# Optimization experiments

Measured on AMD Instinct MI355X. Metric: run time of the kernel, lower is better.

The kernel has to match this reference:

```python
import jax, jax.numpy as jnp
import numpy as np

Q, B, D = 512, 4, 1024      # qlen, batch, d_model
L, H, DH, DI = 4, 16, 64, 4096  # layers, heads, d_head, d_inner
M = 512                      # mem_len


def setup_inputs() -> dict:
    key = jax.random.key(0)
    ks = jax.random.split(key, 10)
    w = lambda i, shape: jax.random.normal(ks[i], shape, jnp.float32) * 0.02
    return dict(
        x=jax.random.normal(ks[0], (Q, B, D), jnp.float32),
        mems=jax.random.normal(ks[1], (L, M, B, D), jnp.float32),
        u=w(2, (H, DH)),
        v=w(3, (H, DH)),
        W_qkv=w(4, (L, D, 3 * H * DH)),
        W_o=w(5, (L, H * DH, D)),
        W_r=w(6, (L, D, H * DH)),
        ln1_g=jnp.ones((L, D), jnp.float32),
        ln1_b=jnp.zeros((L, D), jnp.float32),
        W1=w(7, (L, D, DI)),
        b1=jnp.zeros((L, DI), jnp.float32),
        W2=w(8, (L, DI, D)),
        b2=jnp.zeros((L, D), jnp.float32),
        ln2_g=jnp.ones((L, D), jnp.float32),
        ln2_b=jnp.zeros((L, D), jnp.float32),
    )


def _layer_norm(x, g, b):
    mu = x.mean(-1, keepdims=True)
    var = ((x - mu) ** 2).mean(-1, keepdims=True)
    return (x - mu) * jax.lax.rsqrt(var + 1e-5) * g + b


def _rel_shift(x):
    # x: [q, k, b, n] -> Transformer-XL relative shift
    q, k, b, n = x.shape
    x = jnp.pad(x, ((0, 0), (1, 0), (0, 0), (0, 0)))
    return x.reshape(k + 1, q, b, n)[1:].reshape(q, k, b, n)


def _pos_emb(klen, d):
    pos = jnp.arange(klen - 1, -1, -1.0, dtype=jnp.float32)
    inv_freq = 1.0 / (10000.0 ** (jnp.arange(0, d, 2, dtype=jnp.float32) / d))
    ang = pos[:, None] * inv_freq[None, :]
    return jnp.concatenate([jnp.sin(ang), jnp.cos(ang)], axis=-1)  # [klen, d]


def reference(x, mems, u, v, W_qkv, W_o, W_r, ln1_g, ln1_b, W1, b1, W2, b2, ln2_g, ln2_b):
    q_len, bsz, d = x.shape
    mlen = mems.shape[1]
    klen = mlen + q_len
    r = _pos_emb(klen, d)                       # [klen, d]
    scale = 1.0 / np.sqrt(DH)
    # causal mask with memory: query i may attend key j iff j - i <= mlen
    mask = (jnp.arange(klen)[None, :] - jnp.arange(q_len)[:, None]) > mlen  # [q, k]
    h = x
    for i in range(L):
        cat = jnp.concatenate([mems[i], h], axis=0)       # [klen, b, d]
        heads = cat @ W_qkv[i]                            # [klen, b, 3*H*DH]
        qh, kh, vh = jnp.split(heads, 3, axis=-1)
        qh = qh[-q_len:].reshape(q_len, bsz, H, DH)
        kh = kh.reshape(klen, bsz, H, DH)
        vh = vh.reshape(klen, bsz, H, DH)
        rk = (r @ W_r[i]).reshape(klen, H, DH)            # [klen, H, DH]
        AC = jnp.einsum('ibnd,jbnd->ijbn', qh + u, kh)
        BD = _rel_shift(jnp.einsum('ibnd,jnd->ijbn', qh + v, rk))
        score = (AC + BD) * scale                         # [q, k, b, n]
        score = jnp.where(mask[:, :, None, None], -1e30, score)
        attn = jax.nn.softmax(score, axis=1)
        av = jnp.einsum('ijbn,jbnd->ibnd', attn, vh).reshape(q_len, bsz, H * DH)
        h = _layer_norm(h + av @ W_o[i], ln1_g[i], ln1_b[i])
        ff = jax.nn.relu(h @ W1[i] + b1[i]) @ W2[i] + b2[i]
        h = _layer_norm(h + ff, ln2_g[i], ln2_b[i])
    return h  # [qlen, bsz, d_model]
```

## Files before the change

### kernel.cpp

```cpp
#include <hip/hip_runtime.h>
#include <hip/hip_bf16.h>
#include <cstdint>

#define QL      512
#define BS      4
#define DMODEL  1024
#define NL      4
#define NH      16
#define DHEAD   64
#define DINNER  4096
#define MLEN    512
#define KLEN_   1024
#define HD_     1024
#define THD     3072
#define ROWS_H   2048

typedef __attribute__((ext_vector_type(8))) __bf16 bf16x8;
typedef __attribute__((ext_vector_type(4))) float  f32x4;

enum EpiMode { EPI_F32 = 0, EPI_BF16 = 1, EPI_RELU_BF16 = 2 };

__device__ __forceinline__ void glds16(const void* g, void* l) {
  __builtin_amdgcn_global_load_lds(
      (const __attribute__((address_space(1))) unsigned int*)g,
      (__attribute__((address_space(3))) unsigned int*)l, 16, 0, 0);
}

template<int BM, int BN, int WMT, int WNT, int EPI>
__global__ __launch_bounds__(256) void gemm_bt(
    const __bf16* __restrict__ A, const __bf16* __restrict__ Bt,
    void* __restrict__ Cv, const float* __restrict__ bias,
    int K, int lda, int ldb, int ldc,
    long sA, long Bn, long Cn)
{
  constexpr int WCOLS = BN / (WNT * 16);
  constexpr int WROWS = BM / (WMT * 16);
  static_assert(WCOLS * WROWS == 4, "must be 4 waves");
  __shared__ __align__(16) char smem[(BM + BN) * 64];
  char* sAm = smem;
  char* sBm = smem + BM * 64;

  const int bz = blockIdx.z;
  A  += (size_t)bz * sA;
  Bt += (size_t)bz * Bn;
  const size_t coff = (size_t)bz * Cn;

  const int tid  = threadIdx.x;
  const int wave = tid >> 6, lane = tid & 63;
  const int quad = lane >> 4, mrow = lane & 15;
  const int wr = wave / WCOLS, wc = wave % WCOLS;
  const int bm0 = blockIdx.x * BM, bn0 = blockIdx.y * BN;

  const int srow = lane >> 2;
  const int skq  = (lane & 3) ^ (srow & 3);
  const __bf16* gA = A  + (size_t)(bm0 + wave * (BM / 64) * 16 + srow) * lda + skq * 8;
  const __bf16* gB = Bt + (size_t)(bn0 + wave * (BN / 64) * 16 + srow) * ldb + skq * 8;
  char* lA = sAm + wave * (BM / 64) * 1024;
  char* lB = sBm + wave * (BN / 64) * 1024;

  const int aswz = (quad ^ (mrow & 3)) << 4;

  const f32x4 zero = {0.f, 0.f, 0.f, 0.f};
  f32x4 acc[WMT][WNT];
#pragma unroll
  for (int a = 0; a < WMT; ++a)
#pragma unroll
    for (int b = 0; b < WNT; ++b) acc[a][b] = zero;

  for (int k0 = 0; k0 < K; k0 += 32) {
#pragma unroll
    for (int p = 0; p < BM / 64; ++p)
      glds16(gA + (size_t)p * 16 * lda + k0, lA + p * 1024);
#pragma unroll
    for (int p = 0; p < BN / 64; ++p)
      glds16(gB + (size_t)p * 16 * ldb + k0, lB + p * 1024);
    __syncthreads();
    bf16x8 afr[WMT], bfr[WNT];
#pragma unroll
    for (int mt = 0; mt < WMT; ++mt)
      afr[mt] = *(const bf16x8*)(sAm + (wr * (WMT * 16) + mt * 16 + mrow) * 64 + aswz);
#pragma unroll
    for (int nt = 0; nt < WNT; ++nt)
      bfr[nt] = *(const bf16x8*)(sBm + (wc * (WNT * 16) + nt * 16 + mrow) * 64 + aswz);
#pragma unroll
    for (int mt = 0; mt < WMT; ++mt)
#pragma unroll
      for (int nt = 0; nt < WNT; ++nt)
        acc[mt][nt] = __builtin_amdgcn_mfma_f32_16x16x32_bf16(afr[mt], bfr[nt], acc[mt][nt], 0, 0, 0);
    __syncthreads();
  }

#pragma unroll
  for (int mt = 0; mt < WMT; ++mt) {
#pragma unroll
    for (int nt = 0; nt < WNT; ++nt) {
#pragma unroll
      for (int rr = 0; rr < 4; ++rr) {
        int gm = bm0 + wr * (WMT * 16) + mt * 16 + quad * 4 + rr;
        int gn = bn0 + wc * (WNT * 16) + nt * 16 + mrow;
        float val = acc[mt][nt][rr];
        if constexpr (EPI == EPI_F32) {
          ((float*)Cv)[coff + (size_t)gm * ldc + gn] = val;
        } else if constexpr (EPI == EPI_BF16) {
          ((__bf16*)Cv)[coff + (size_t)gm * ldc + gn] = (__bf16)val;
        } else {
          val += bias[gn];
          ((__bf16*)Cv)[coff + (size_t)gm * ldc + gn] = (__bf16)fmaxf(val, 0.f);
        }
      }
    }
  }
}

__global__ __launch_bounds__(256) void flash_attn(
    const __bf16* __restrict__ qu,
    const __bf16* __restrict__ qv,
    const __bf16* __restrict__ heads,
    const __bf16* __restrict__ rk,
    const __bf16* __restrict__ vt,
    __bf16* __restrict__ av)
{
  __shared__ __align__(16) char kh_t[64 * 144];
  __shared__ __align__(16) char rv_t[64 * 144];
  __shared__ __align__(16) char p_t [64 * 144];
  __shared__ float raw[64 * 132];

  const int t   = blockIdx.x;
  const int i0  = t * 64;
  const int bn  = blockIdx.y;
  const int b   = bn >> 4, n = bn & 15;
  const int tid = threadIdx.x;
  const int wave = tid >> 6, lane = tid & 63;
  const int quad = lane >> 4, mrow = lane & 15;
  const f32x4 zero = {0.f, 0.f, 0.f, 0.f};

  const __bf16* qub = qu + (size_t)bn * QL * DHEAD;
  const __bf16* qvb = qv + (size_t)bn * QL * DHEAD;
  const int qrow = i0 + wave * 16 + mrow;
  bf16x8 quf0 = *(const bf16x8*)(qub + (size_t)qrow * 64 + quad * 8);
  bf16x8 quf1 = *(const bf16x8*)(qub + (size_t)qrow * 64 + 32 + quad * 8);
  bf16x8 qvf0 = *(const bf16x8*)(qvb + (size_t)qrow * 64 + quad * 8);
  bf16x8 qvf1 = *(const bf16x8*)(qvb + (size_t)qrow * 64 + 32 + quad * 8);

  f32x4 o[4];
#pragma unroll
  for (int dt = 0; dt < 4; ++dt) o[dt] = zero;
  float m_r[4], l_r[4];
#pragma unroll
  for (int rr = 0; rr < 4; ++rr) { m_r[rr] = -3.0e38f; l_r[rr] = 0.f; }

  const int sr = tid >> 3;
  const int sc = (tid & 7) * 8;

  const int c0 = 448 - i0;
#pragma unroll
  for (int p = 0; p < 2; ++p) {
    int r = p * 32 + sr;
    bf16x8 vv = *(const bf16x8*)(rk + (size_t)(c0 + r) * HD_ + n * 64 + sc);
    *(bf16x8*)(rv_t + r * 144 + sc * 2) = vv;
  }
  __syncthreads();
  {
    int slot = ((c0 >> 6) & 1) * 64;
#pragma unroll
    for (int ct = 0; ct < 4; ++ct) {
      bf16x8 b0 = *(const bf16x8*)(rv_t + (ct * 16 + mrow) * 144 + quad * 16);
      bf16x8 b1 = *(const bf16x8*)(rv_t + (ct * 16 + mrow) * 144 + 64 + quad * 16);
      f32x4 r = __builtin_amdgcn_mfma_f32_16x16x32_bf16(qvf0, b0, zero, 0, 0, 0);
      r = __builtin_amdgcn_mfma_f32_16x16x32_bf16(qvf1, b1, r, 0, 0, 0);
#pragma unroll
      for (int rr = 0; rr < 4; ++rr)
        raw[(wave * 16 + quad * 4 + rr) * 132 + slot + ct * 16 + mrow] = r[rr];
    }
  }
  __syncthreads();

  const int i_base = i0 + wave * 16 + quad * 4;
  const int nt = t + 9;
  for (int k = 0; k < nt; ++k) {
    const int j0 = k * 64;
#pragma unroll
    for (int p = 0; p < 2; ++p) {
      int r = p * 32 + sr;
      bf16x8 kv = *(const bf16x8*)(heads + (size_t)((j0 + r) * BS + b) * THD + HD_ + n * 64 + sc);
      *(bf16x8*)(kh_t + r * 144 + sc * 2) = kv;
    }
    const int c0n = c0 + 64 * (k + 1);
    if (c0n < KLEN_) {
#pragma unroll
      for (int p = 0; p < 2; ++p) {
        int r = p * 32 + sr;
        bf16x8 rv = *(const bf16x8*)(rk + (size_t)(c0n + r) * HD_ + n * 64 + sc);
        *(bf16x8*)(rv_t + r * 144 + sc * 2) = rv;
      }
    }
    __syncthreads();
    if (c0n < KLEN_) {
      int slot = ((c0n >> 6) & 1) * 64;
#pragma unroll
      for (int ct = 0; ct < 4; ++ct) {
        bf16x8 b0 = *(const bf16x8*)(rv_t + (ct * 16 + mrow) * 144 + quad * 16);
        bf16x8 b1 = *(const bf16x8*)(rv_t + (ct * 16 + mrow) * 144 + 64 + quad * 16);
        f32x4 r = __builtin_amdgcn_mfma_f32_16x16x32_bf16(qvf0, b0, zero, 0, 0, 0);
        r = __builtin_amdgcn_mfma_f32_16x16x32_bf16(qvf1, b1, r, 0, 0, 0);
#pragma unroll
        for (int rr = 0; rr < 4; ++rr)
          raw[(wave * 16 + quad * 4 + rr) * 132 + slot + ct * 16 + mrow] = r[rr];
      }
    }
    f32x4 s[4];
#pragma unroll
    for (int ct = 0; ct < 4; ++ct) {
      bf16x8 b0 = *(const bf16x8*)(kh_t + (ct * 16 + mrow) * 144 + quad * 16);
      bf16x8 b1 = *(const bf16x8*)(kh_t + (ct * 16 + mrow) * 144 + 64 + quad * 16);
      s[ct] = __builtin_amdgcn_mfma_f32_16x16x32_bf16(quf0, b0, zero, 0, 0, 0);
      s[ct] = __builtin_amdgcn_mfma_f32_16x16x32_bf16(quf1, b1, s[ct], 0, 0, 0);
    }
    __syncthreads();
#pragma unroll
    for (int p = 0; p < 2; ++p) {
      int r = p * 32 + sr;
      bf16x8 vv = *(const bf16x8*)(vt + (size_t)bn * (DHEAD * KLEN_) + (size_t)r * KLEN_ + j0 + sc);
      *(bf16x8*)(rv_t + r * 144 + sc * 2) = vv;
    }
#pragma unroll
    for (int ct = 0; ct < 4; ++ct) {
#pragma unroll
      for (int rr = 0; rr < 4; ++rr) {
        int i = i_base + rr;
        int j = j0 + ct * 16 + mrow;
        float val;
        if (j - i <= MLEN) {
          int c = j - i + (QL - 1);
          int col = ((c >> 6) & 1) * 64 + (c & 63);
          val = (s[ct][rr] + raw[(wave * 16 + quad * 4 + rr) * 132 + col]) * 0.125f;
        } else val = -3.0e38f;
        s[ct][rr] = val;
      }
    }
    float alpha[4];
#pragma unroll
    for (int rr = 0; rr < 4; ++rr) {
      float mx = fmaxf(fmaxf(s[0][rr], s[1][rr]), fmaxf(s[2][rr], s[3][rr]));
#pragma unroll
      for (int off = 1; off < 16; off <<= 1) mx = fmaxf(mx, __shfl_xor(mx, off));
      float m_new = fmaxf(m_r[rr], mx);
      alpha[rr] = __expf(m_r[rr] - m_new);
      m_r[rr] = m_new;
      float rs = 0.f;
#pragma unroll
      for (int ct = 0; ct < 4; ++ct) {
        float pv = __expf(s[ct][rr] - m_new);
        s[ct][rr] = pv;
        rs += pv;
      }
#pragma unroll
      for (int off = 1; off < 16; off <<= 1) rs += __shfl_xor(rs, off);
      l_r[rr] = l_r[rr] * alpha[rr] + rs;
    }
#pragma unroll
    for (int dt = 0; dt < 4; ++dt)
#pragma unroll
      for (int rr = 0; rr < 4; ++rr) o[dt][rr] *= alpha[rr];
#pragma unroll
    for (int ct = 0; ct < 4; ++ct)
#pragma unroll
      for (int rr = 0; rr < 4; ++rr)
        ((__bf16*)p_t)[(wave * 16 + quad * 4 + rr) * 72 + ct * 16 + mrow] = (__bf16)s[ct][rr];
    __syncthreads();
    {
      bf16x8 pf0 = *(const bf16x8*)(p_t + (wave * 16 + mrow) * 144 + quad * 16);
      bf16x8 pf1 = *(const bf16x8*)(p_t + (wave * 16 + mrow) * 144 + 64 + quad * 16);
#pragma unroll
      for (int dt = 0; dt < 4; ++dt) {
        bf16x8 vf0 = *(const bf16x8*)(rv_t + (dt * 16 + mrow) * 144 + quad * 16);
        bf16x8 vf1 = *(const bf16x8*)(rv_t + (dt * 16 + mrow) * 144 + 64 + quad * 16);
        o[dt] = __builtin_amdgcn_mfma_f32_16x16x32_bf16(pf0, vf0, o[dt], 0, 0, 0);
        o[dt] = __builtin_amdgcn_mfma_f32_16x16x32_bf16(pf1, vf1, o[dt], 0, 0, 0);
      }
    }
    __syncthreads();
  }

#pragma unroll
  for (int dt = 0; dt < 4; ++dt) {
#pragma unroll
    for (int rr = 0; rr < 4; ++rr) {
      int i = i_base + rr;
      float outv = o[dt][rr] / l_r[rr];
      av[((size_t)i * BS + b) * HD_ + n * 64 + dt * 16 + mrow] = (__bf16)outv;
    }
  }
}


__global__ __launch_bounds__(256) void transpose_f32_bf16(
    const float* __restrict__ in, unsigned short* __restrict__ out, int R, int C)
{
  __shared__ float tile[64][66];
  int c0 = blockIdx.x * 64, r0 = blockIdx.y * 64;
  int tx = threadIdx.x, ty = threadIdx.y;
#pragma unroll
  for (int s = 0; s < 8; ++s) {
    int r = ty + s * 8;
    const float* p = in + (size_t)(r0 + r) * C + c0 + 2 * tx;
    tile[r][2 * tx]     = p[0];
    tile[r][2 * tx + 1] = p[1];
  }
  __syncthreads();
#pragma unroll
  for (int s = 0; s < 8; ++s) {
    int c = ty + s * 8;
    __bf16 lo = (__bf16)tile[2 * tx][c];
    __bf16 hi = (__bf16)tile[2 * tx + 1][c];
    unsigned int w = (unsigned int)*(unsigned short*)&lo |
                     ((unsigned int)*(unsigned short*)&hi << 16);
    *(unsigned int*)(out + (size_t)(c0 + c) * R + r0 + 2 * tx) = w;
  }
}

__global__ __launch_bounds__(256) void cast_f32_bf16(const float* __restrict__ in,
                                                     __bf16* __restrict__ out, int n)
{
  int i = blockIdx.x * 256 + threadIdx.x;
  if (i < n) out[i] = (__bf16)in[i];
}

__global__ __launch_bounds__(256) void posemb_kernel(__bf16* __restrict__ r)
{
  int idx = blockIdx.x * 256 + threadIdx.x;
  int p = idx >> 10, c = idx & 1023;
  int t = c & 511;
  float invf = __expf(-((float)t / 512.0f) * 9.210340371976184f);
  float ang = (float)(KLEN_ - 1 - p) * invf;
  float val = (c < 512) ? sinf(ang) : cosf(ang);
  r[idx] = (__bf16)val;
}

__global__ __launch_bounds__(256) void init_h(const float* __restrict__ x,
                                              float* __restrict__ hm,
                                              __bf16* __restrict__ hbf, int n)
{
  int i = blockIdx.x * 256 + threadIdx.x;
  if (i < n) { float t = x[i]; hm[i] = t; hbf[i] = (__bf16)t; }
}

__global__ __launch_bounds__(256) void build_quqv(const __bf16* __restrict__ heads,
                                                  const float* __restrict__ u,
                                                  const float* __restrict__ v,
                                                  __bf16* __restrict__ qu,
                                                  __bf16* __restrict__ qv)
{
  int idx = blockIdx.x * 256 + threadIdx.x;
  int d = idx & 63;
  int i = (idx >> 6) & (QL - 1);
  int bn = idx >> 15;
  int b = bn >> 4, n = bn & 15;
  float q = (float)heads[(size_t)((MLEN + i) * BS + b) * THD + n * 64 + d];
  int ud = n * 64 + d;
  qu[idx] = (__bf16)(q + u[ud]);
  qv[idx] = (__bf16)(q + v[ud]);
}

__global__ __launch_bounds__(256) void build_vt(const unsigned short* __restrict__ heads,
                                                unsigned short* __restrict__ vt)
{
  __shared__ unsigned short tile[64][65];
  int bn = blockIdx.y; int b = bn >> 4, n = bn & 15;
  int j0 = blockIdx.x * 64;
  int tx = threadIdx.x, ty = threadIdx.y;
#pragma unroll
  for (int s = 0; s < 16; ++s) {
    int j = ty + s * 4;
    tile[j][tx] = heads[(size_t)((j0 + j) * BS + b) * THD + 2048 + n * 64 + tx];
  }
  __syncthreads();
#pragma unroll
  for (int s = 0; s < 16; ++s) {
    int d = ty + s * 4;
    vt[(size_t)bn * DHEAD * KLEN_ + (size_t)d * KLEN_ + j0 + tx] = tile[tx][d];
  }
}

__global__ __launch_bounds__(256) void ln_kernel(float* __restrict__ hm,
                                                 const float* __restrict__ d0,
                                                 const float* __restrict__ d1,
                                                 const float* __restrict__ bias,
                                                 const float* __restrict__ g,
                                                 const float* __restrict__ b,
                                                 __bf16* __restrict__ hbf,
                                                 float* __restrict__ outf)
{
  int row = blockIdx.x;
  size_t base = (size_t)row * DMODEL;
  int tid = threadIdx.x;
  float x[4]; float sum = 0.f, sq = 0.f;
#pragma unroll
  for (int p = 0; p < 4; ++p) {
    int c = p * 256 + tid;
    float t = hm[base + c] + d0[base + c];
    if (d1) t += d1[base + c];
    if (bias) t += bias[c];
    x[p] = t; sum += t; sq += t * t;
  }
#pragma unroll
  for (int off = 32; off > 0; off >>= 1) { sum += __shfl_xor(sum, off); sq += __shfl_xor(sq, off); }
  __shared__ float rs[4], rq[4];
  int wave = tid >> 6, lane = tid & 63;
  if (lane == 0) { rs[wave] = sum; rq[wave] = sq; }
  __syncthreads();
  sum = rs[0] + rs[1] + rs[2] + rs[3];
  sq  = rq[0] + rq[1] + rq[2] + rq[3];
  float mu  = sum * (1.0f / DMODEL);
  float var = sq * (1.0f / DMODEL) - mu * mu;
  float rstd = rsqrtf(var + 1e-5f);
#pragma unroll
  for (int p = 0; p < 4; ++p) {
    int c = p * 256 + tid;
    float y = (x[p] - mu) * rstd * g[c] + b[c];
    hm[base + c] = y;
    hbf[base + c] = (__bf16)y;
    if (outf) outf[base + c] = y;
  }
}

extern "C" void kernel_launch(void* const* d_in, const int* in_sizes, int n_in,
                              void* d_out, int out_size, void* d_ws, size_t ws_size,
                              hipStream_t stream) {
  (void)in_sizes; (void)n_in; (void)out_size; (void)ws_size;
  const float* x    = (const float*)d_in[0];
  const float* mems = (const float*)d_in[1];
  const float* u    = (const float*)d_in[2];
  const float* v    = (const float*)d_in[3];
  const float* Wqkv = (const float*)d_in[4];
  const float* Wo   = (const float*)d_in[5];
  const float* Wr   = (const float*)d_in[6];
  const float* ln1g = (const float*)d_in[7];
  const float* ln1b = (const float*)d_in[8];
  const float* W1   = (const float*)d_in[9];
  const float* b1   = (const float*)d_in[10];
  const float* W2   = (const float*)d_in[11];
  const float* b2   = (const float*)d_in[12];
  const float* ln2g = (const float*)d_in[13];
  const float* ln2b = (const float*)d_in[14];

  size_t off = 0;
  char* ws = (char*)d_ws;
  auto alloc = [&](size_t bytes) { size_t o = off; off += (bytes + 255) & ~(size_t)255; return o; };
  __bf16* wT    = (__bf16*)(ws + alloc((size_t)DINNER * DMODEL * 2));
  char*   R1    = (char*)(ws + alloc((size_t)(2 * ROWS_H) * THD * 2));
  __bf16* heads = (__bf16*)R1;
  float*  proj  = (float*)R1;
  __bf16* ff1   = (__bf16*)(R1 + (size_t)ROWS_H * DMODEL * 4);
  __bf16* catb  = (__bf16*)(ws + alloc((size_t)(2 * ROWS_H) * DMODEL * 2));
  __bf16* memsb = catb;
  __bf16* hbf   = catb + (size_t)ROWS_H * DMODEL;
  __bf16* av    = catb;
  __bf16* r_bf  = (__bf16*)(ws + alloc((size_t)KLEN_ * DMODEL * 2));
  __bf16* rk4   = (__bf16*)(ws + alloc((size_t)NL * KLEN_ * HD_ * 2));
  __bf16* qu    = (__bf16*)(ws + alloc((size_t)2 * BS * NH * QL * DHEAD * 2));
  __bf16* qv    = qu + (size_t)BS * NH * QL * DHEAD;
  float*  ff2p  = (float*)qu;
  __bf16* vt    = (__bf16*)(ws + alloc((size_t)BS * NH * DHEAD * KLEN_ * 2));
  float*  hm    = (float*)(ws + alloc((size_t)ROWS_H * DMODEL * 4));

  posemb_kernel<<<(KLEN_ * DMODEL) / 256, 256, 0, stream>>>(r_bf);
  init_h<<<(ROWS_H * DMODEL) / 256, 256, 0, stream>>>(x, hm, hbf, ROWS_H * DMODEL);

  for (int i = 0; i < NL; ++i)
    transpose_f32_bf16<<<dim3(HD_ / 64, DMODEL / 64), dim3(32, 8), 0, stream>>>(
        Wr + (size_t)i * DMODEL * HD_, (unsigned short*)(wT + (size_t)i * HD_ * DMODEL),
        DMODEL, HD_);
  gemm_bt<128, 128, 4, 4, EPI_BF16><<<dim3(8, 8, NL), 256, 0, stream>>>(
      r_bf, wT, rk4, nullptr, DMODEL, DMODEL, DMODEL, HD_,
      0, (long)HD_ * DMODEL, (long)KLEN_ * HD_);

  for (int i = 0; i < NL; ++i) {
    cast_f32_bf16<<<(MLEN * BS * DMODEL) / 256, 256, 0, stream>>>(
        mems + (size_t)i * MLEN * BS * DMODEL, memsb, MLEN * BS * DMODEL);
    transpose_f32_bf16<<<dim3(THD / 64, DMODEL / 64), dim3(32, 8), 0, stream>>>(
        Wqkv + (size_t)i * DMODEL * THD, (unsigned short*)wT, DMODEL, THD);
    gemm_bt<128, 128, 4, 4, EPI_BF16><<<dim3(32, 24, 1), 256, 0, stream>>>(
        catb, wT, heads, nullptr, DMODEL, DMODEL, DMODEL, THD, 0, 0, 0);

    build_quqv<<<(BS * NH * QL * DHEAD) / 256, 256, 0, stream>>>(heads, u, v, qu, qv);
    build_vt<<<dim3(KLEN_ / 64, BS * NH), dim3(64, 4), 0, stream>>>(
        (const unsigned short*)heads, (unsigned short*)vt);

    flash_attn<<<dim3(8, 64), 256, 0, stream>>>(
        qu, qv, heads, rk4 + (size_t)i * KLEN_ * HD_, vt, av);

    transpose_f32_bf16<<<dim3(DMODEL / 64, HD_ / 64), dim3(32, 8), 0, stream>>>(
        Wo + (size_t)i * HD_ * DMODEL, (unsigned short*)wT, HD_, DMODEL);
    gemm_bt<128, 64, 4, 2, EPI_F32><<<dim3(16, 16, 1), 256, 0, stream>>>(
        av, wT, proj, nullptr, HD_, HD_, HD_, DMODEL, 0, 0, 0);
    ln_kernel<<<ROWS_H, 256, 0, stream>>>(hm, proj, nullptr, nullptr,
                                          ln1g + i * DMODEL, ln1b + i * DMODEL, hbf, nullptr);

    transpose_f32_bf16<<<dim3(DINNER / 64, DMODEL / 64), dim3(32, 8), 0, stream>>>(
        W1 + (size_t)i * DMODEL * DINNER, (unsigned short*)wT, DMODEL, DINNER);
    gemm_bt<128, 128, 4, 4, EPI_RELU_BF16><<<dim3(16, 32, 1), 256, 0, stream>>>(
        hbf, wT, ff1, b1 + i * DINNER, DMODEL, DMODEL, DMODEL, DINNER, 0, 0, 0);

    transpose_f32_bf16<<<dim3(DMODEL / 64, DINNER / 64), dim3(32, 8), 0, stream>>>(
        W2 + (size_t)i * DINNER * DMODEL, (unsigned short*)wT, DINNER, DMODEL);
    gemm_bt<128, 64, 4, 2, EPI_F32><<<dim3(16, 16, 2), 256, 0, stream>>>(
        ff1, wT, proj, nullptr, DINNER / 2, DINNER, DINNER, DMODEL,
        (long)(DINNER / 2), (long)(DINNER / 2), (long)(ff2p - proj));
    ln_kernel<<<ROWS_H, 256, 0, stream>>>(hm, proj, ff2p, b2 + i * DMODEL,
                                          ln2g + i * DMODEL, ln2b + i * DMODEL, hbf,
                                          (i == NL - 1) ? (float*)d_out : nullptr);
  }
}
```

Baseline: 1.226 ms.

## Split attention KV range across two workgroups with combine kernel and XCD-aware mapping

Each (batch, head, query-tile) is split into two workgroups that process halves of the key range, writing normalized partial outputs plus max and sum stats. A new combine kernel merges the partials with log-sum-exp weights. The launch grid is flattened so blocks of one bn share an XCD, which targets L2 locality. The change also adds s_setprio around the MFMA sections and reuses kh_t for P to cut LDS. It doubles occupancy on a grid that was only 512 blocks, in exchange for an extra kernel launch, bf16 partial round-trips and workspace aliasing (avp reuses wT, mlprt reuses hbf).

```diff
diff --git a/kernel.cpp b/kernel.cpp
--- a/kernel.cpp
+++ b/kernel.cpp
@@ -16,6 +16,7 @@
 #define ROWS_H   2048
 
 typedef __attribute__((ext_vector_type(8))) __bf16 bf16x8;
+typedef __attribute__((ext_vector_type(4))) __bf16 bf16x4;
 typedef __attribute__((ext_vector_type(4))) float  f32x4;
 
 enum EpiMode { EPI_F32 = 0, EPI_BF16 = 1, EPI_RELU_BF16 = 2 };
@@ -118,17 +119,27 @@
     const __bf16* __restrict__ heads,
     const __bf16* __restrict__ rk,
     const __bf16* __restrict__ vt,
-    __bf16* __restrict__ av)
+    __bf16* __restrict__ avp,
+    float* __restrict__ mlpart)
 {
   __shared__ __align__(16) char kh_t[64 * 144];
   __shared__ __align__(16) char rv_t[64 * 144];
-  __shared__ __align__(16) char p_t [64 * 144];
   __shared__ float raw[64 * 132];
 
-  const int t   = blockIdx.x;
-  const int i0  = t * 64;
-  const int bn  = blockIdx.y;
-  const int b   = bn >> 4, n = bn & 15;
+  const int wgid = blockIdx.x;
+  const int xcd  = wgid & 7;
+  const int slotw = wgid >> 3;
+  const int bn   = ((slotw >> 4) << 3) + xcd;
+  const int inner = slotw & 15;
+  const int t    = inner & 7;
+  const int z    = inner >> 3;
+  const int i0   = t * 64;
+  const int b    = bn >> 4, n = bn & 15;
+  const int nt   = t + 9;
+  const int h    = (nt + 1) >> 1;
+  const int ks   = z ? h : 0;
+  const int ke   = z ? nt : h;
+
   const int tid = threadIdx.x;
   const int wave = tid >> 6, lane = tid & 63;
   const int quad = lane >> 4, mrow = lane & 15;
@@ -153,15 +164,17 @@
   const int sc = (tid & 7) * 8;
 
   const int c0 = 448 - i0;
+  const int cpre = c0 + 64 * ks;
 #pragma unroll
   for (int p = 0; p < 2; ++p) {
     int r = p * 32 + sr;
-    bf16x8 vv = *(const bf16x8*)(rk + (size_t)(c0 + r) * HD_ + n * 64 + sc);
+    bf16x8 vv = *(const bf16x8*)(rk + (size_t)(cpre + r) * HD_ + n * 64 + sc);
     *(bf16x8*)(rv_t + r * 144 + sc * 2) = vv;
   }
   __syncthreads();
   {
-    int slot = ((c0 >> 6) & 1) * 64;
+    int slotc = ((cpre >> 6) & 1) * 64;
+    __builtin_amdgcn_s_setprio(1);
 #pragma unroll
     for (int ct = 0; ct < 4; ++ct) {
       bf16x8 b0 = *(const bf16x8*)(rv_t + (ct * 16 + mrow) * 144 + quad * 16);
@@ -170,14 +183,14 @@
       r = __builtin_amdgcn_mfma_f32_16x16x32_bf16(qvf1, b1, r, 0, 0, 0);
 #pragma unroll
       for (int rr = 0; rr < 4; ++rr)
-        raw[(wave * 16 + quad * 4 + rr) * 132 + slot + ct * 16 + mrow] = r[rr];
-    }
+        raw[(wave * 16 + quad * 4 + rr) * 132 + slotc + ct * 16 + mrow] = r[rr];
+    }
+    __builtin_amdgcn_s_setprio(0);
   }
   __syncthreads();
 
   const int i_base = i0 + wave * 16 + quad * 4;
-  const int nt = t + 9;
-  for (int k = 0; k < nt; ++k) {
+  for (int k = ks; k < ke; ++k) {
     const int j0 = k * 64;
 #pragma unroll
     for (int p = 0; p < 2; ++p) {
@@ -195,8 +208,9 @@
       }
     }
     __syncthreads();
+    __builtin_amdgcn_s_setprio(1);
     if (c0n < KLEN_) {
-      int slot = ((c0n >> 6) & 1) * 64;
+      int slotc = ((c0n >> 6) & 1) * 64;
 #pragma unroll
       for (int ct = 0; ct < 4; ++ct) {
         bf16x8 b0 = *(const bf16x8*)(rv_t + (ct * 16 + mrow) * 144 + quad * 16);
@@ -205,7 +219,7 @@
         r = __builtin_amdgcn_mfma_f32_16x16x32_bf16(qvf1, b1, r, 0, 0, 0);
 #pragma unroll
         for (int rr = 0; rr < 4; ++rr)
-          raw[(wave * 16 + quad * 4 + rr) * 132 + slot + ct * 16 + mrow] = r[rr];
+          raw[(wave * 16 + quad * 4 + rr) * 132 + slotc + ct * 16 + mrow] = r[rr];
       }
     }
     f32x4 s[4];
@@ -216,6 +230,7 @@
       s[ct] = __builtin_amdgcn_mfma_f32_16x16x32_bf16(quf0, b0, zero, 0, 0, 0);
       s[ct] = __builtin_amdgcn_mfma_f32_16x16x32_bf16(quf1, b1, s[ct], 0, 0, 0);
     }
+    __builtin_amdgcn_s_setprio(0);
     __syncthreads();
 #pragma unroll
     for (int p = 0; p < 2; ++p) {
@@ -266,11 +281,12 @@
     for (int ct = 0; ct < 4; ++ct)
 #pragma unroll
       for (int rr = 0; rr < 4; ++rr)
-        ((__bf16*)p_t)[(wave * 16 + quad * 4 + rr) * 72 + ct * 16 + mrow] = (__bf16)s[ct][rr];
+        ((__bf16*)kh_t)[(wave * 16 + quad * 4 + rr) * 72 + ct * 16 + mrow] = (__bf16)s[ct][rr];
     __syncthreads();
     {
-      bf16x8 pf0 = *(const bf16x8*)(p_t + (wave * 16 + mrow) * 144 + quad * 16);
-      bf16x8 pf1 = *(const bf16x8*)(p_t + (wave * 16 + mrow) * 144 + 64 + quad * 16);
+      bf16x8 pf0 = *(const bf16x8*)(kh_t + (wave * 16 + mrow) * 144 + quad * 16);
+      bf16x8 pf1 = *(const bf16x8*)(kh_t + (wave * 16 + mrow) * 144 + 64 + quad * 16);
+      __builtin_amdgcn_s_setprio(1);
 #pragma unroll
       for (int dt = 0; dt < 4; ++dt) {
         bf16x8 vf0 = *(const bf16x8*)(rv_t + (dt * 16 + mrow) * 144 + quad * 16);
@@ -278,19 +294,54 @@
         o[dt] = __builtin_amdgcn_mfma_f32_16x16x32_bf16(pf0, vf0, o[dt], 0, 0, 0);
         o[dt] = __builtin_amdgcn_mfma_f32_16x16x32_bf16(pf1, vf1, o[dt], 0, 0, 0);
       }
+      __builtin_amdgcn_s_setprio(0);
     }
     __syncthreads();
   }
 
-#pragma unroll
-  for (int dt = 0; dt < 4; ++dt) {
+  const size_t prow = ((size_t)z * 64 + bn) * 512;
+#pragma unroll
+  for (int rr = 0; rr < 4; ++rr) {
+    int i = i_base + rr;
+    float inv = 1.0f / l_r[rr];
+#pragma unroll
+    for (int dt = 0; dt < 4; ++dt)
+      avp[(prow + i) * 64 + dt * 16 + mrow] = (__bf16)(o[dt][rr] * inv);
+  }
+  if (mrow == 0) {
 #pragma unroll
     for (int rr = 0; rr < 4; ++rr) {
       int i = i_base + rr;
-      float outv = o[dt][rr] / l_r[rr];
-      av[((size_t)i * BS + b) * HD_ + n * 64 + dt * 16 + mrow] = (__bf16)outv;
-    }
-  }
+      mlpart[(prow + i) * 2]     = m_r[rr];
+      mlpart[(prow + i) * 2 + 1] = l_r[rr];
+    }
+  }
+}
+
+__global__ __launch_bounds__(256) void attn_combine(
+    const __bf16* __restrict__ avp, const float* __restrict__ mlpart,
+    __bf16* __restrict__ av)
+{
+  int idx = blockIdx.x * 256 + threadIdx.x;
+  int dq = idx & 15;
+  int i  = (idx >> 4) & 511;
+  int bn = idx >> 13;
+  int b = bn >> 4, n = bn & 15;
+  size_t r0 = (size_t)bn * 512 + i;
+  size_t r1 = r0 + (size_t)64 * 512;
+  float m1 = mlpart[r0 * 2], l1 = mlpart[r0 * 2 + 1];
+  float m2 = mlpart[r1 * 2], l2 = mlpart[r1 * 2 + 1];
+  float m  = fmaxf(m1, m2);
+  float w1 = l1 * __expf(m1 - m), w2 = l2 * __expf(m2 - m);
+  float inv = 1.0f / (w1 + w2);
+  w1 *= inv; w2 *= inv;
+  bf16x4 o1 = *(const bf16x4*)(avp + r0 * 64 + dq * 4);
+  bf16x4 o2 = *(const bf16x4*)(avp + r1 * 64 + dq * 4);
+  bf16x4 ov;
+#pragma unroll
+  for (int j = 0; j < 4; ++j)
+    ov[j] = (__bf16)((float)o1[j] * w1 + (float)o2[j] * w2);
+  *(bf16x4*)(av + ((size_t)i * BS + b) * HD_ + n * 64 + dq * 4) = ov;
 }
 
 
@@ -456,6 +507,8 @@
   __bf16* memsb = catb;
   __bf16* hbf   = catb + (size_t)ROWS_H * DMODEL;
   __bf16* av    = catb;
+  float*  mlprt = (float*)hbf;
+  __bf16* avp   = wT;
   __bf16* r_bf  = (__bf16*)(ws + alloc((size_t)KLEN_ * DMODEL * 2));
   __bf16* rk4   = (__bf16*)(ws + alloc((size_t)NL * KLEN_ * HD_ * 2));
   __bf16* qu    = (__bf16*)(ws + alloc((size_t)2 * BS * NH * QL * DHEAD * 2));
@@ -487,8 +540,9 @@
     build_vt<<<dim3(KLEN_ / 64, BS * NH), dim3(64, 4), 0, stream>>>(
         (const unsigned short*)heads, (unsigned short*)vt);
 
-    flash_attn<<<dim3(8, 64), 256, 0, stream>>>(
-        qu, qv, heads, rk4 + (size_t)i * KLEN_ * HD_, vt, av);
+    flash_attn<<<dim3(1024), 256, 0, stream>>>(
+        qu, qv, heads, rk4 + (size_t)i * KLEN_ * HD_, vt, avp, mlprt);
+    attn_combine<<<(64 * 512 * 16) / 256, 256, 0, stream>>>(avp, mlprt, av);
 
     transpose_f32_bf16<<<dim3(DMODEL / 64, HD_ / 64), dim3(32, 8), 0, stream>>>(
         Wo + (size_t)i * HD_ * DMODEL, (unsigned short*)wT, HD_, DMODEL);
```

Result: no change. 1.228 ms (+0.2%).
